# Optimization experiments

Hardware: AMD Instinct MI355X
Metric: run time of the kernel (lower is better)

## Reference

```python
import jax, jax.numpy as jnp
import numpy as np

I, H, O = 512, 1024, 2  # input_size, hidden_size, output_size
B, S = 64, 512          # batch, seq_len


def setup_inputs() -> dict:
    key = jax.random.key(0)
    ks = jax.random.split(key, 9)
    sc = 1.0 / np.sqrt(I + H)
    return {
        "x": jax.random.normal(ks[0], (B, S, I), dtype=jnp.float32),
        "h": jnp.zeros((B, 1, H), dtype=jnp.float32),
        "Wz": jax.random.uniform(ks[1], (I + H, H), jnp.float32, -sc, sc),
        "bz": jax.random.uniform(ks[2], (H,), jnp.float32, -sc, sc),
        "Wr": jax.random.uniform(ks[3], (I + H, H), jnp.float32, -sc, sc),
        "br": jax.random.uniform(ks[4], (H,), jnp.float32, -sc, sc),
        "Wh": jax.random.uniform(ks[5], (I + H, H), jnp.float32, -sc, sc),
        "bh": jax.random.uniform(ks[6], (H,), jnp.float32, -sc, sc),
        "Wfc": jax.random.uniform(ks[7], (H, O), jnp.float32, -1.0 / np.sqrt(H), 1.0 / np.sqrt(H)),
        "bfc": jax.random.uniform(ks[8], (O,), jnp.float32, -1.0 / np.sqrt(H), 1.0 / np.sqrt(H)),
    }


def reference(x, h, Wz, bz, Wr, br, Wh, bh, Wfc, bfc):
    h0 = jnp.squeeze(h, axis=1)  # (B, H)

    def step(hid, xt):  # xt: (B, I), hid: (B, H)
        ih = jnp.concatenate([xt, hid], axis=1)              # (B, I+H)
        z = jax.nn.sigmoid(ih @ Wz + bz)                     # update gate
        r = jax.nn.sigmoid(ih @ Wr + br)                     # reset gate
        ihr = jnp.concatenate([xt, r * hid], axis=1)
        h_cand = jnp.tanh(ihr @ Wh + bh)
        new_h = (1.0 - z) * hid + z * h_cand
        return new_h, None

    x_t = jnp.transpose(x, (1, 0, 2))  # (S, B, I)
    h_last, _ = jax.lax.scan(step, h0, x_t)
    out = jax.nn.relu(h_last) @ Wfc + bfc  # (B, O)
    return jax.nn.log_softmax(out, axis=1)
```

## Files before the change

kernel.cpp:

```cpp
#include <hip/hip_runtime.h>

typedef __attribute__((ext_vector_type(4))) short bf4;
typedef __attribute__((ext_vector_type(8))) short bf8;
typedef __attribute__((ext_vector_type(4))) float f4;

#define BB 64
#define SS 512
#define II 512
#define HH 1024
#define SCH 64
#define NCH 8
#define GBLK 64

__device__ __forceinline__ short f2bf(float f) {
  unsigned u = __float_as_uint(f);
  u = u + 0x7fff + ((u >> 16) & 1);
  return (short)(u >> 16);
}
__device__ __forceinline__ float bf2f(short s) {
  return __uint_as_float(((unsigned)(unsigned short)s) << 16);
}
__device__ __forceinline__ float sigm(float x) {
  return 1.0f / (1.0f + __expf(-x));
}
__device__ __forceinline__ float tanh_f(float x) {
  float e = __expf(-2.0f * fabsf(x));
  float t = (1.0f - e) / (1.0f + e);
  return copysignf(t, x);
}


__global__ __launch_bounds__(256) void cast_x_k(const float* __restrict__ x, short* __restrict__ xb) {
  size_t i = ((size_t)blockIdx.x * 256 + threadIdx.x) * 4;
  float4 v = *(const float4*)(x + i);
  bf4 o; o[0] = f2bf(v.x); o[1] = f2bf(v.y); o[2] = f2bf(v.z); o[3] = f2bf(v.w);
  *(bf4*)(xb + i) = o;
}

__global__ __launch_bounds__(256) void prep_wxt_k(const float* __restrict__ Wz, const float* __restrict__ Wr,
                                                  const float* __restrict__ Wh, short* __restrict__ WxT) {
  int idx = blockIdx.x * 256 + threadIdx.x;
  int g = idx >> 19;
  int rem = idx & 524287;
  int n = rem >> 9, k = rem & 511;
  const float* W = (g == 0) ? Wz : (g == 1) ? Wr : Wh;
  WxT[idx] = f2bf(W[(size_t)k * HH + n]);
}

__global__ __launch_bounds__(256) void prep_uswz_k(const float* __restrict__ Wz, const float* __restrict__ Wr,
                                                   const float* __restrict__ Wh, short* __restrict__ Us) {
  int t = blockIdx.x * 256 + threadIdx.x;
  int lane = t & 63, kk = (t >> 6) & 31, nb = (t >> 11) & 63, g = t >> 17;
  const float* W = (g == 0) ? Wz : (g == 1) ? Wr : Wh;
  int n = nb * 16 + (lane & 15);
  int kb = II + kk * 32 + (lane >> 4) * 8;
  bf8 o;
#pragma unroll
  for (int j = 0; j < 8; j++) o[j] = f2bf(W[(size_t)(kb + j) * HH + n]);
  *(bf8*)(Us + (size_t)t * 8) = o;
}

__global__ __launch_bounds__(256) void init_h_k(const float* __restrict__ h, float* __restrict__ h32,
                                                short* __restrict__ hb) {
  int i = blockIdx.x * 256 + threadIdx.x;
  float v = h[i];
  h32[i] = v; hb[i] = f2bf(v);
}

__global__ __launch_bounds__(256) void gemm_k(const short* __restrict__ xb, const short* __restrict__ WxT,
                                              const float* __restrict__ bz, const float* __restrict__ br,
                                              const float* __restrict__ bh, short* __restrict__ Gx, int s0) {
  __shared__ short Al[4 * 64 * 8];
  __shared__ short Bl[4 * 64 * 8];
  int tid = threadIdx.x, wave = tid >> 6, lane = tid & 63;
  int sl = blockIdx.x;
  int n0 = blockIdx.y * 64;
  f4 acc[4] = {};
  int mp = tid >> 2, q = tid & 3;
  const short* asrc = xb + ((size_t)mp * SS + (s0 + sl)) * II + q * 8;
  int ng = n0 + mp;
  int gb = ng >> 10, hb_ = ng & 1023;
  const short* bsrc = WxT + ((size_t)gb * HH + hb_) * II + q * 8;
  int adst = ((mp >> 4) * 64 + q * 16 + (mp & 15)) * 8;

  for (int kk = 0; kk < II; kk += 32) {
    bf8 av = *(const bf8*)(asrc + kk);
    bf8 bv = *(const bf8*)(bsrc + kk);
    __syncthreads();
    *(bf8*)&Al[adst] = av;
    *(bf8*)&Bl[adst] = bv;
    __syncthreads();
    bf8 af = *(bf8*)&Al[(wave * 64 + lane) * 8];
#pragma unroll
    for (int ns = 0; ns < 4; ns++) {
      bf8 bfr = *(bf8*)&Bl[(ns * 64 + lane) * 8];
      acc[ns] = __builtin_amdgcn_mfma_f32_16x16x32_bf16(af, bfr, acc[ns], 0, 0, 0);
    }
  }
  int brow0 = wave * 16 + (lane >> 4) * 4;
#pragma unroll
  for (int ns = 0; ns < 4; ns++) {
    int ngl = n0 + ns * 16 + (lane & 15);
    int g2 = ngl >> 10, h2 = ngl & 1023;
    float bias = ((g2 == 0) ? bz : (g2 == 1) ? br : bh)[h2];
    bf4 o;
#pragma unroll
    for (int i = 0; i < 4; i++) o[i] = f2bf(acc[ns][i] + bias);
    *(bf4*)&Gx[(((size_t)sl * 3 + g2) * HH + h2) * BB + brow0] = o;
  }
}


__device__ __forceinline__ void gbar(unsigned* flags, unsigned target) {
  __syncthreads();
  if (threadIdx.x == 0)
    __hip_atomic_store(&flags[blockIdx.x], target, __ATOMIC_RELEASE, __HIP_MEMORY_SCOPE_AGENT);
  if (threadIdx.x < GBLK) {
    while (__hip_atomic_load(&flags[threadIdx.x], __ATOMIC_ACQUIRE, __HIP_MEMORY_SCOPE_AGENT) < target)
      __builtin_amdgcn_s_sleep(2);
  }
  __syncthreads();
}

__global__ __launch_bounds__(256) void rec_k(const short* __restrict__ Gx, const short* __restrict__ Us,
                                             float* __restrict__ h32, short* __restrict__ hb,
                                             short* __restrict__ rhb, unsigned* __restrict__ flags) {
  __shared__ short Uzr[2 * 32 * 64 * 8];
  int tid = threadIdx.x, wave = tid >> 6, lane = tid & 63, bid = blockIdx.x;
  {
    const bf8* sz = (const bf8*)Us + ((size_t)(0 * 64 + bid)) * 2048;
    const bf8* sr = (const bf8*)Us + ((size_t)(1 * 64 + bid)) * 2048;
    bf8* d = (bf8*)Uzr;
    for (int i = tid; i < 2048; i += 256) { d[i] = sz[i]; d[2048 + i] = sr[i]; }
  }
  const bf8* Uh = (const bf8*)Us + ((size_t)(2 * 64 + bid)) * 2048;

  int n0 = bid * 16;
  int brow0 = wave * 16 + (lane >> 4) * 4;
  int ncol = n0 + (lane & 15);
  float hreg[4];
#pragma unroll
  for (int i = 0; i < 4; i++) hreg[i] = h32[(size_t)(brow0 + i) * HH + ncol];
  __syncthreads();

  const short* hrow  = hb  + ((size_t)(wave * 16 + (lane & 15))) * HH + (lane >> 4) * 8;
  const short* rhrow = rhb + ((size_t)(wave * 16 + (lane & 15))) * HH + (lane >> 4) * 8;

  unsigned target = 0;
  for (int t = 0; t < SCH; t++) {
    f4 zacc = {}, racc = {};
#pragma unroll 8
    for (int kk = 0; kk < 32; kk++) {
      bf8 af = *(const bf8*)(hrow + kk * 32);
      bf8 b0 = *(bf8*)&Uzr[(kk * 64 + lane) * 8];
      zacc = __builtin_amdgcn_mfma_f32_16x16x32_bf16(af, b0, zacc, 0, 0, 0);
      bf8 b1 = *(bf8*)&Uzr[(2048 + kk * 64 + lane) * 8];
      racc = __builtin_amdgcn_mfma_f32_16x16x32_bf16(af, b1, racc, 0, 0, 0);
    }
    const short* gz = Gx + (((size_t)t * 3 + 0) * HH + ncol) * BB + brow0;
    bf4 gzv = *(const bf4*)gz;
    bf4 grv = *(const bf4*)(gz + (size_t)HH * BB);
    float zf[4];
#pragma unroll
    for (int i = 0; i < 4; i++) {
      zf[i] = sigm(zacc[i] + bf2f(gzv[i]));
      float r = sigm(racc[i] + bf2f(grv[i]));
      rhb[(size_t)(brow0 + i) * HH + ncol] = f2bf(r * hreg[i]);
    }
    gbar(flags, ++target);
    f4 cacc = {};
#pragma unroll 8
    for (int kk = 0; kk < 32; kk++) {
      bf8 af = *(const bf8*)(rhrow + kk * 32);
      bf8 b2 = Uh[kk * 64 + lane];
      cacc = __builtin_amdgcn_mfma_f32_16x16x32_bf16(af, b2, cacc, 0, 0, 0);
    }
    bf4 ghv = *(const bf4*)(Gx + (((size_t)t * 3 + 2) * HH + ncol) * BB + brow0);
#pragma unroll
    for (int i = 0; i < 4; i++) {
      float c = tanh_f(cacc[i] + bf2f(ghv[i]));
      float hn = hreg[i] + zf[i] * (c - hreg[i]);
      hreg[i] = hn;
      hb[(size_t)(brow0 + i) * HH + ncol] = f2bf(hn);
    }
    gbar(flags, ++target);
  }
#pragma unroll
  for (int i = 0; i < 4; i++) h32[(size_t)(brow0 + i) * HH + ncol] = hreg[i];
}


__global__ __launch_bounds__(64) void out_k(const float* __restrict__ h32, const float* __restrict__ Wfc,
                                            const float* __restrict__ bfc, float* __restrict__ out) {
  int b = blockIdx.x, t = threadIdx.x;
  float a0 = 0.f, a1 = 0.f;
  for (int k = t; k < HH; k += 64) {
    float hv = fmaxf(h32[(size_t)b * HH + k], 0.f);
    a0 += hv * Wfc[k * 2]; a1 += hv * Wfc[k * 2 + 1];
  }
#pragma unroll
  for (int off = 32; off > 0; off >>= 1) { a0 += __shfl_down(a0, off); a1 += __shfl_down(a1, off); }
  if (t == 0) {
    float y0 = a0 + bfc[0], y1 = a1 + bfc[1];
    float m = fmaxf(y0, y1);
    float lse = m + logf(__expf(y0 - m) + __expf(y1 - m));
    out[b * 2] = y0 - lse; out[b * 2 + 1] = y1 - lse;
  }
}


extern "C" void kernel_launch(void* const* d_in, const int* in_sizes, int n_in,
                              void* d_out, int out_size, void* d_ws, size_t ws_size,
                              hipStream_t stream) {
  const float* x   = (const float*)d_in[0];
  const float* h0  = (const float*)d_in[1];
  const float* Wz  = (const float*)d_in[2];
  const float* bz  = (const float*)d_in[3];
  const float* Wr  = (const float*)d_in[4];
  const float* br  = (const float*)d_in[5];
  const float* Wh  = (const float*)d_in[6];
  const float* bh  = (const float*)d_in[7];
  const float* Wfc = (const float*)d_in[8];
  const float* bfc = (const float*)d_in[9];
  float* out = (float*)d_out;

  char* ws = (char*)d_ws;
  short*    xb    = (short*)(ws);
  short*    WxT   = (short*)(ws + 33554432);
  short*    Us    = (short*)(ws + 36700160);
  short*    Gx    = (short*)(ws + 42991616);
  float*    h32   = (float*)(ws + 68157440);
  short*    hbuf  = (short*)(ws + 68419584);
  short*    rhb   = (short*)(ws + 68550656);
  unsigned* flags = (unsigned*)(ws + 68681728);

  cast_x_k<<<16384, 256, 0, stream>>>(x, xb);
  prep_wxt_k<<<6144, 256, 0, stream>>>(Wz, Wr, Wh, WxT);
  prep_uswz_k<<<1536, 256, 0, stream>>>(Wz, Wr, Wh, Us);
  init_h_k<<<256, 256, 0, stream>>>(h0, h32, hbuf);

  for (int c = 0; c < NCH; c++) {
    gemm_k<<<dim3(SCH, 48), 256, 0, stream>>>(xb, WxT, bz, br, bh, Gx, c * SCH);
    hipMemsetAsync(flags, 0, GBLK * sizeof(unsigned), stream);
    rec_k<<<GBLK, 256, 0, stream>>>(Gx, Us, h32, hbuf, rhb, flags);
  }
  out_k<<<BB, 64, 0, stream>>>(h32, Wfc, bfc, out);
}
```

Measured before the change: 11.72 ms.

## Use relaxed agent-scope atomics for shared hidden-state exchange and lighten grid barrier

Reads and writes of the shared hidden-state buffers now go through relaxed agent-scope atomic loads and stores. The intent is to keep them coherent at device level so the barrier's acquire can become a relaxed poll with a shorter sleep. Stores are packed into 32-bit pairs via a lane shuffle, A-fragment loads are batched eight at a time ahead of the MFMAs, and the candidate-gate Gx load is hoisted to the top of the step. This risks memory-ordering bugs, because the plain __syncthreads barrier no longer carries acquire semantics for other data.

```diff
diff --git a/kernel.cpp b/kernel.cpp
--- a/kernel.cpp
+++ b/kernel.cpp
@@ -27,6 +27,13 @@
   float e = __expf(-2.0f * fabsf(x));
   float t = (1.0f - e) / (1.0f + e);
   return copysignf(t, x);
+}
+
+__device__ __forceinline__ unsigned long long ld_u64_l3(const unsigned long long* p) {
+  return __hip_atomic_load((unsigned long long*)p, __ATOMIC_RELAXED, __HIP_MEMORY_SCOPE_AGENT);
+}
+__device__ __forceinline__ void st_u32_l3(unsigned* p, unsigned v) {
+  __hip_atomic_store(p, v, __ATOMIC_RELAXED, __HIP_MEMORY_SCOPE_AGENT);
 }
 
 
@@ -116,15 +123,18 @@
   if (threadIdx.x == 0)
     __hip_atomic_store(&flags[blockIdx.x], target, __ATOMIC_RELEASE, __HIP_MEMORY_SCOPE_AGENT);
   if (threadIdx.x < GBLK) {
-    while (__hip_atomic_load(&flags[threadIdx.x], __ATOMIC_ACQUIRE, __HIP_MEMORY_SCOPE_AGENT) < target)
-      __builtin_amdgcn_s_sleep(2);
-  }
+    while (__hip_atomic_load(&flags[threadIdx.x], __ATOMIC_RELAXED, __HIP_MEMORY_SCOPE_AGENT) < target)
+      __builtin_amdgcn_s_sleep(1);
+  }
+  __asm__ volatile("" ::: "memory");
   __syncthreads();
 }
 
+union HL { unsigned long long u[2]; bf8 v; };
+
 __global__ __launch_bounds__(256) void rec_k(const short* __restrict__ Gx, const short* __restrict__ Us,
-                                             float* __restrict__ h32, short* __restrict__ hb,
-                                             short* __restrict__ rhb, unsigned* __restrict__ flags) {
+                                             float* __restrict__ h32, short* hb,
+                                             short* rhb, unsigned* flags) {
   __shared__ short Uzr[2 * 32 * 64 * 8];
   int tid = threadIdx.x, wave = tid >> 6, lane = tid & 63, bid = blockIdx.x;
   {
@@ -143,45 +153,72 @@
   for (int i = 0; i < 4; i++) hreg[i] = h32[(size_t)(brow0 + i) * HH + ncol];
   __syncthreads();
 
-  const short* hrow  = hb  + ((size_t)(wave * 16 + (lane & 15))) * HH + (lane >> 4) * 8;
-  const short* rhrow = rhb + ((size_t)(wave * 16 + (lane & 15))) * HH + (lane >> 4) * 8;
+  size_t aoff = ((size_t)(wave * 16 + (lane & 15)) * HH + (lane >> 4) * 8) / 4;
+  const unsigned long long* hq  = (const unsigned long long*)hb  + aoff;
+  const unsigned long long* rhq = (const unsigned long long*)rhb + aoff;
 
   unsigned target = 0;
   for (int t = 0; t < SCH; t++) {
-    f4 zacc = {}, racc = {};
-#pragma unroll 8
-    for (int kk = 0; kk < 32; kk++) {
-      bf8 af = *(const bf8*)(hrow + kk * 32);
-      bf8 b0 = *(bf8*)&Uzr[(kk * 64 + lane) * 8];
-      zacc = __builtin_amdgcn_mfma_f32_16x16x32_bf16(af, b0, zacc, 0, 0, 0);
-      bf8 b1 = *(bf8*)&Uzr[(2048 + kk * 64 + lane) * 8];
-      racc = __builtin_amdgcn_mfma_f32_16x16x32_bf16(af, b1, racc, 0, 0, 0);
-    }
     const short* gz = Gx + (((size_t)t * 3 + 0) * HH + ncol) * BB + brow0;
     bf4 gzv = *(const bf4*)gz;
     bf4 grv = *(const bf4*)(gz + (size_t)HH * BB);
+    bf4 ghv = *(const bf4*)(gz + 2 * (size_t)HH * BB);
+    f4 zacc = {}, racc = {};
+#pragma unroll
+    for (int g = 0; g < 4; g++) {
+      HL a[8];
+#pragma unroll
+      for (int j = 0; j < 8; j++) {
+        int kk = g * 8 + j;
+        a[j].u[0] = ld_u64_l3(hq + kk * 8);
+        a[j].u[1] = ld_u64_l3(hq + kk * 8 + 1);
+      }
+#pragma unroll
+      for (int j = 0; j < 8; j++) {
+        int kk = g * 8 + j;
+        bf8 b0 = *(bf8*)&Uzr[(kk * 64 + lane) * 8];
+        zacc = __builtin_amdgcn_mfma_f32_16x16x32_bf16(a[j].v, b0, zacc, 0, 0, 0);
+        bf8 b1 = *(bf8*)&Uzr[(2048 + kk * 64 + lane) * 8];
+        racc = __builtin_amdgcn_mfma_f32_16x16x32_bf16(a[j].v, b1, racc, 0, 0, 0);
+      }
+    }
     float zf[4];
 #pragma unroll
     for (int i = 0; i < 4; i++) {
       zf[i] = sigm(zacc[i] + bf2f(gzv[i]));
       float r = sigm(racc[i] + bf2f(grv[i]));
-      rhb[(size_t)(brow0 + i) * HH + ncol] = f2bf(r * hreg[i]);
+      unsigned sv = (unsigned)(unsigned short)f2bf(r * hreg[i]);
+      unsigned up = __shfl_down(sv, 1);
+      if (!(lane & 1))
+        st_u32_l3((unsigned*)rhb + ((size_t)(brow0 + i) * HH + ncol) / 2, sv | (up << 16));
     }
     gbar(flags, ++target);
     f4 cacc = {};
-#pragma unroll 8
-    for (int kk = 0; kk < 32; kk++) {
-      bf8 af = *(const bf8*)(rhrow + kk * 32);
-      bf8 b2 = Uh[kk * 64 + lane];
-      cacc = __builtin_amdgcn_mfma_f32_16x16x32_bf16(af, b2, cacc, 0, 0, 0);
-    }
-    bf4 ghv = *(const bf4*)(Gx + (((size_t)t * 3 + 2) * HH + ncol) * BB + brow0);
+#pragma unroll
+    for (int g = 0; g < 4; g++) {
+      HL a[8];
+#pragma unroll
+      for (int j = 0; j < 8; j++) {
+        int kk = g * 8 + j;
+        a[j].u[0] = ld_u64_l3(rhq + kk * 8);
+        a[j].u[1] = ld_u64_l3(rhq + kk * 8 + 1);
+      }
+#pragma unroll
+      for (int j = 0; j < 8; j++) {
+        int kk = g * 8 + j;
+        bf8 b2 = Uh[kk * 64 + lane];
+        cacc = __builtin_amdgcn_mfma_f32_16x16x32_bf16(a[j].v, b2, cacc, 0, 0, 0);
+      }
+    }
 #pragma unroll
     for (int i = 0; i < 4; i++) {
       float c = tanh_f(cacc[i] + bf2f(ghv[i]));
       float hn = hreg[i] + zf[i] * (c - hreg[i]);
       hreg[i] = hn;
-      hb[(size_t)(brow0 + i) * HH + ncol] = f2bf(hn);
+      unsigned sv = (unsigned)(unsigned short)f2bf(hn);
+      unsigned up = __shfl_down(sv, 1);
+      if (!(lane & 1))
+        st_u32_l3((unsigned*)hb + ((size_t)(brow0 + i) * HH + ncol) / 2, sv | (up << 16));
     }
     gbar(flags, ++target);
   }
```

Result: no change. 11.65 ms (-0.6%).
